# Optimization experiments

Measured on AMD Instinct MI355X. Metric: run time of the kernel, lower is better.

## Reference

```python
import jax, jax.numpy as jnp
import numpy as np

D_MODEL = 1024
NUM_HEADS = 16
HEAD_WIDTH = 64
SEQ_LEN = 2048
BATCH = 2
NEG_INF = -1e9


def alibi_slopes(num_heads):
    # 2**(-i * 8/num_heads) for i = 1..num_heads, shape [H, 1, 1]
    step = 8.0 / num_heads
    i = jnp.arange(1, num_heads + 1, dtype=jnp.float32)
    return (2.0 ** (-i * step))[:, None, None]


def relative_positions(t_q, t_v):
    # matrix[i, j] = j - i, shape [t_q, t_v]
    return (jnp.arange(t_v)[None, :] - jnp.arange(t_q)[:, None]).astype(jnp.float32)


def setup_inputs() -> dict:
    key = jax.random.key(0)
    ks = jax.random.split(key, 6)
    queries = jax.random.normal(ks[0], (BATCH, SEQ_LEN, D_MODEL), dtype=jnp.float32)
    keys = jax.random.normal(ks[1], (BATCH, SEQ_LEN, D_MODEL), dtype=jnp.float32)
    values = jax.random.normal(ks[2], (BATCH, SEQ_LEN, D_MODEL), dtype=jnp.float32)
    # causal additive mask, broadcastable [1, 1, S, S]
    causal = jnp.where(
        jnp.arange(SEQ_LEN)[None, :] > jnp.arange(SEQ_LEN)[:, None], NEG_INF, 0.0
    ).astype(jnp.float32)[None, None]
    scale = 1.0 / np.sqrt(D_MODEL)
    Wq = jax.random.normal(ks[3], (D_MODEL, D_MODEL), dtype=jnp.float32) * scale
    Wk = jax.random.normal(ks[4], (D_MODEL, D_MODEL), dtype=jnp.float32) * scale
    Wv = jax.random.normal(ks[5], (D_MODEL, D_MODEL), dtype=jnp.float32) * scale
    return {"queries": queries, "keys": keys, "values": values, "mask": causal,
            "Wq": Wq, "Wk": Wk, "Wv": Wv}


def reference(queries, keys, values, mask, Wq, Wk, Wv):
    N, t_q, d = queries.shape
    _, t_v, _ = keys.shape
    H, hw = NUM_HEADS, HEAD_WIDTH

    def split_heads(x, t):
        # [N, t, d] -> [N, H, t, hw]  (nn.Linear: x @ W.T)
        return x.reshape(N, t, H, hw).transpose(0, 2, 1, 3)

    q = split_heads(queries @ Wq.T, t_q)
    k = split_heads(keys @ Wk.T, t_v)
    v = split_heads(values @ Wv.T, t_v)

    att = jnp.einsum("bhqd,bhkd->bhqk", q, k) / np.sqrt(hw)
    # ALiBi bias: slope_h * (j - i), broadcast over batch
    att = att + (alibi_slopes(H) * relative_positions(t_q, t_v))[None]
    att = att + mask[:, :, :t_q, :t_v]
    att = jax.nn.softmax(att, axis=-1)
    res = jnp.einsum("bhqk,bhkd->bhqd", att, v)  # [N, H, t_q, hw]
    return res.transpose(0, 2, 1, 3).reshape(N, t_v, d)
```

## Files before the change

### kernel.cpp

```cpp
#include <hip/hip_runtime.h>
#include <hip/hip_bf16.h>

#define BATCH 2
#define HEADS 16
#define SEQ 2048
#define HW 64
#define DMODEL 1024

typedef unsigned short u16;
typedef __attribute__((ext_vector_type(8))) short short8;
typedef __attribute__((ext_vector_type(4))) float floatx4;

typedef __attribute__((address_space(3))) void* lds_t;
typedef const __attribute__((address_space(1))) void* gbl_t;

__device__ __forceinline__ u16 f2bf(float f) {
    union { float f; unsigned int u; } v; v.f = f;
    unsigned int r = v.u + 0x7fffu + ((v.u >> 16) & 1u);
    return (u16)(r >> 16);
}

__device__ __forceinline__ unsigned int pk2bf(float a, float b) {
    union { __hip_bfloat162 h; unsigned int u; } c;
    c.h = __float22bfloat162_rn(make_float2(a, b));
    return c.u;
}

__global__ __launch_bounds__(256) void proj_kernel(
    const float* __restrict__ Xk, const float* __restrict__ Xv, const float* __restrict__ Xq,
    const float* __restrict__ Wk, const float* __restrict__ Wv, const float* __restrict__ Wq,
    u16* __restrict__ Ok, u16* __restrict__ Ov, u16* __restrict__ Oq)
{
    const float* X; const float* W;
    if (blockIdx.z == 0)      { X = Xk; W = Wk; }
    else if (blockIdx.z == 1) { X = Xv; W = Wv; }
    else                      { X = Xq; W = Wq; }

    __shared__ u16 As[128][72];
    __shared__ u16 Bs[128][72];

    const int tid = threadIdx.x;
    const int lane = tid & 63, wave = tid >> 6;
    const int quad = lane >> 4, l15 = lane & 15;
    const int wm = (wave >> 1) << 6, wn = (wave & 1) << 6;
    const int tm = blockIdx.y, tn = blockIdx.x;

    const int sr = tid >> 4;
    const int sc = (tid & 15) << 2;
    const float* Xp = X + (size_t)(tm * 128 + sr) * DMODEL + sc;
    const float* Wp = W + (size_t)(tn * 128 + sr) * DMODEL + sc;

    float4 ra[8], rb[8];
#define PLOAD(K0) \
    for (int i = 0; i < 8; i++) { \
        ra[i] = *reinterpret_cast<const float4*>(Xp + (size_t)16 * i * DMODEL + (K0)); \
        rb[i] = *reinterpret_cast<const float4*>(Wp + (size_t)16 * i * DMODEL + (K0)); \
    }

    floatx4 acc[4][4];
    for (int i = 0; i < 4; i++) for (int j = 0; j < 4; j++) acc[i][j] = (floatx4)0.0f;

    PLOAD(0);
    for (int k0 = 0; k0 < DMODEL; k0 += 64) {
        for (int i = 0; i < 8; i++) {
            uint2 pa; pa.x = pk2bf(ra[i].x, ra[i].y); pa.y = pk2bf(ra[i].z, ra[i].w);
            *reinterpret_cast<uint2*>(&As[sr + 16 * i][sc]) = pa;
            uint2 pb; pb.x = pk2bf(rb[i].x, rb[i].y); pb.y = pk2bf(rb[i].z, rb[i].w);
            *reinterpret_cast<uint2*>(&Bs[sr + 16 * i][sc]) = pb;
        }
        __syncthreads();
        if (k0 + 64 < DMODEL) { PLOAD(k0 + 64); }
        for (int kc = 0; kc < 2; kc++) {
            short8 af[4], bf[4];
            for (int i = 0; i < 4; i++)
                af[i] = *reinterpret_cast<const short8*>(&As[wm + i * 16 + l15][kc * 32 + quad * 8]);
            for (int j = 0; j < 4; j++)
                bf[j] = *reinterpret_cast<const short8*>(&Bs[wn + j * 16 + l15][kc * 32 + quad * 8]);
            for (int i = 0; i < 4; i++)
                for (int j = 0; j < 4; j++)
                    acc[i][j] = __builtin_amdgcn_mfma_f32_16x16x32_bf16(af[i], bf[j], acc[i][j], 0, 0, 0);
        }
        __syncthreads();
    }
#undef PLOAD

    if (blockIdx.z != 1) {
        u16* O = (blockIdx.z == 0) ? Ok : Oq;
        const float mul = (blockIdx.z == 0) ? 1.0f : 0.125f;
        for (int i = 0; i < 4; i++) for (int j = 0; j < 4; j++) {
            int n = (tn << 7) + wn + (j << 4) + l15;
            int h = n >> 6, d = n & 63;
            for (int r = 0; r < 4; r++) {
                int m = (tm << 7) + wm + (i << 4) + (quad << 2) + r;
                int b = m >> 11, s = m & 2047;
                int pc = (((d >> 3) ^ (s & 7)) << 3) | (d & 7);
                O[(size_t)((((b << 4) + h) << 11) + s) * 64 + pc] = f2bf(acc[i][j][r] * mul);
            }
        }
    } else {
        for (int i = 0; i < 4; i++) for (int j = 0; j < 4; j++) {
            int n = (tn << 7) + wn + (j << 4) + l15;
            int h = n >> 6, d = n & 63;
            int m = (tm << 7) + wm + (i << 4) + (quad << 2);
            int b = m >> 11, s0 = m & 2047;
            int ps = (s0 & ~63) | (((((s0 >> 3) & 7) ^ (d & 7)) << 3)) | (s0 & 7);
            uint2 pk;
            pk.x = pk2bf(acc[i][j][0], acc[i][j][1]);
            pk.y = pk2bf(acc[i][j][2], acc[i][j][3]);
            *reinterpret_cast<uint2*>(Ov + ((size_t)(((b << 4) + h) << 6) + d) * SEQ + ps) = pk;
        }
    }
}

__global__ __launch_bounds__(256) void attn_kernel(
    const u16* __restrict__ Qg, const u16* __restrict__ K,
    const u16* __restrict__ VtG, float* __restrict__ out)
{
    __shared__ u16 smem[16896];
    u16* Pst = smem + 12288;

    const int tid = threadIdx.x;
    const int lane = tid & 63, wave = tid >> 6;
    const int quad = lane >> 4, l15 = lane & 15;

    const int bid = blockIdx.x;
    const int qt = 31 - (bid >> 5);
    const int bh = bid & 31;
    const int b = bh >> 4, h = bh & 15;
    const float slope = exp2f(-0.5f * (float)(h + 1));
    const int q0 = qt << 6;
    const int swz = l15 & 7;

    const u16* Qh  = Qg  + (size_t)bh * SEQ * HW;
    const u16* Kh  = K   + (size_t)bh * SEQ * HW;
    const u16* Vth = VtG + (size_t)bh * HW * SEQ;

#define ISSUE_K(KV, BUF) do { \
    const u16* gk_ = Kh + (size_t)((KV) + wave * 16) * 64 + lane * 8; \
    __builtin_amdgcn_global_load_lds((gbl_t)gk_, (lds_t)(smem + (BUF) * 4096 + wave * 1024), 16, 0, 0); \
    __builtin_amdgcn_global_load_lds((gbl_t)(gk_ + 512), (lds_t)(smem + (BUF) * 4096 + wave * 1024 + 512), 16, 0, 0); \
} while (0)
#define ISSUE_V(KV) do { \
    const u16* gv_ = Vth + (size_t)(wave * 16 + (lane >> 3)) * SEQ + (KV) + (lane & 7) * 8; \
    __builtin_amdgcn_global_load_lds((gbl_t)gv_, (lds_t)(smem + 8192 + wave * 1024), 16, 0, 0); \
    __builtin_amdgcn_global_load_lds((gbl_t)(gv_ + 8 * SEQ), (lds_t)(smem + 8192 + wave * 1024 + 512), 16, 0, 0); \
} while (0)

    {
        const u16* gq = Qh + (size_t)(q0 + wave * 16) * 64 + lane * 8;
        __builtin_amdgcn_global_load_lds((gbl_t)gq, (lds_t)(smem + 8192 + wave * 1024), 16, 0, 0);
        __builtin_amdgcn_global_load_lds((gbl_t)(gq + 512), (lds_t)(smem + 8192 + wave * 1024 + 512), 16, 0, 0);
    }
    asm volatile("s_waitcnt vmcnt(0)" ::: "memory");
    short8 qf[2];
    qf[0] = *reinterpret_cast<const short8*>(smem + 8192 + (wave * 16 + l15) * 64 + ((quad ^ swz) << 3));
    qf[1] = *reinterpret_cast<const short8*>(smem + 8192 + (wave * 16 + l15) * 64 + (((quad + 4) ^ swz) << 3));
    asm volatile("s_waitcnt lgkmcnt(0)" ::: "memory");
    __builtin_amdgcn_sched_barrier(0);

    ISSUE_K(0, 0);

    const float L2E = 1.44269504088896340736f;
    const float MB  = 12.0f * L2E;
    const int qg = q0 + (wave << 4) + l15;
    const float SL = slope * L2E;

    float lpart = 0.0f;
    floatx4 acc_o[4];
    for (int t = 0; t < 4; t++) acc_o[t] = (floatx4)0.0f;

    for (int kt = 0; kt <= qt; kt++) {
        const int kv0 = kt << 6;
        asm volatile("s_waitcnt vmcnt(0)" ::: "memory");
        __builtin_amdgcn_s_barrier();
        __builtin_amdgcn_sched_barrier(0);
        ISSUE_V(kv0);
        if (kt < qt) { ISSUE_K(kv0 + 64, (kt + 1) & 1); }

        const u16* Kbase = smem + (kt & 1) * 4096;
        floatx4 sv[4];
        __builtin_amdgcn_s_setprio(1);
        for (int t = 0; t < 4; t++) {
            short8 kf0 = *reinterpret_cast<const short8*>(Kbase + (t * 16 + l15) * 64 + ((quad ^ swz) << 3));
            short8 kf1 = *reinterpret_cast<const short8*>(Kbase + (t * 16 + l15) * 64 + (((quad + 4) ^ swz) << 3));
            floatx4 s = (floatx4)0.0f;
            s = __builtin_amdgcn_mfma_f32_16x16x32_bf16(kf0, qf[0], s, 0, 0, 0);
            s = __builtin_amdgcn_mfma_f32_16x16x32_bf16(kf1, qf[1], s, 0, 0, 0);
            sv[t] = s;
        }
        __builtin_amdgcn_s_setprio(0);

        u16* Pt = Pst + wave * 1152;
        if (kt < qt) {
            const float b0 = fmaf(SL, (float)(kv0 + (quad << 2) - qg), -MB);
            for (int t = 0; t < 4; t++) {
                float p0 = __builtin_amdgcn_exp2f(fmaf(sv[t][0], L2E, fmaf(SL, (float)(t * 16 + 0), b0)));
                float p1 = __builtin_amdgcn_exp2f(fmaf(sv[t][1], L2E, fmaf(SL, (float)(t * 16 + 1), b0)));
                float p2 = __builtin_amdgcn_exp2f(fmaf(sv[t][2], L2E, fmaf(SL, (float)(t * 16 + 2), b0)));
                float p3 = __builtin_amdgcn_exp2f(fmaf(sv[t][3], L2E, fmaf(SL, (float)(t * 16 + 3), b0)));
                lpart += (p0 + p1) + (p2 + p3);
                uint2 pk; pk.x = pk2bf(p0, p1); pk.y = pk2bf(p2, p3);
                *reinterpret_cast<uint2*>(Pt + l15 * 72 + t * 16 + (quad << 2)) = pk;
            }
        } else {
            const float fb = (float)(kv0 + (quad << 2) - qg);
            for (int t = 0; t < 4; t++) {
                float p[4];
                for (int r = 0; r < 4; r++) {
                    float rel = fb + (float)(t * 16 + r);
                    float bd = fmaf(fminf(slope * rel, -1e9f * rel), L2E, -MB);
                    p[r] = __builtin_amdgcn_exp2f(fmaf(sv[t][r], L2E, bd));
                }
                lpart += (p[0] + p[1]) + (p[2] + p[3]);
                uint2 pk; pk.x = pk2bf(p[0], p[1]); pk.y = pk2bf(p[2], p[3]);
                *reinterpret_cast<uint2*>(Pt + l15 * 72 + t * 16 + (quad << 2)) = pk;
            }
        }

        if (kt < qt) { asm volatile("s_waitcnt vmcnt(2)" ::: "memory"); }
        else         { asm volatile("s_waitcnt vmcnt(0)" ::: "memory"); }
        __builtin_amdgcn_s_barrier();
        __builtin_amdgcn_sched_barrier(0);

        short8 pf0 = *reinterpret_cast<const short8*>(Pt + l15 * 72 + quad * 8);
        short8 pf1 = *reinterpret_cast<const short8*>(Pt + l15 * 72 + 32 + quad * 8);
        __builtin_amdgcn_s_setprio(1);
        for (int t2 = 0; t2 < 4; t2++) {
            short8 vf0 = *reinterpret_cast<const short8*>(smem + 8192 + (t2 * 16 + l15) * 64 + ((quad ^ swz) << 3));
            short8 vf1 = *reinterpret_cast<const short8*>(smem + 8192 + (t2 * 16 + l15) * 64 + (((quad + 4) ^ swz) << 3));
            acc_o[t2] = __builtin_amdgcn_mfma_f32_16x16x32_bf16(vf0, pf0, acc_o[t2], 0, 0, 0);
            acc_o[t2] = __builtin_amdgcn_mfma_f32_16x16x32_bf16(vf1, pf1, acc_o[t2], 0, 0, 0);
        }
        __builtin_amdgcn_s_setprio(0);
    }
#undef ISSUE_K
#undef ISSUE_V

    float l_run = lpart;
    l_run += __shfl_xor(l_run, 16);
    l_run += __shfl_xor(l_run, 32);
    const float inv = 1.0f / l_run;

    float* op = out + (size_t)(b * SEQ + qg) * DMODEL + h * 64;
    for (int t2 = 0; t2 < 4; t2++) {
        float4 o;
        o.x = acc_o[t2][0] * inv; o.y = acc_o[t2][1] * inv;
        o.z = acc_o[t2][2] * inv; o.w = acc_o[t2][3] * inv;
        *reinterpret_cast<float4*>(op + t2 * 16 + (quad << 2)) = o;
    }
}

extern "C" void kernel_launch(void* const* d_in, const int* in_sizes, int n_in,
                              void* d_out, int out_size, void* d_ws, size_t ws_size,
                              hipStream_t stream) {
    const float* q  = (const float*)d_in[0];
    const float* k  = (const float*)d_in[1];
    const float* v  = (const float*)d_in[2];
    const float* wq = (const float*)d_in[4];
    const float* wk = (const float*)d_in[5];
    const float* wv = (const float*)d_in[6];
    float* out = (float*)d_out;

    const size_t headElems = (size_t)BATCH * HEADS * SEQ * HW;
    u16* Kb  = (u16*)d_ws;
    u16* VtB = Kb + headElems;
    u16* Qb  = VtB + headElems;

    dim3 pgrid(DMODEL / 128, (BATCH * SEQ) / 128, 3);
    proj_kernel<<<pgrid, 256, 0, stream>>>(k, v, q, wk, wv, wq, Kb, VtB, Qb);
    attn_kernel<<<BATCH * HEADS * (SEQ / 64), 256, 0, stream>>>(Qb, Kb, VtB, out);
}
```

Measured before the change: 206.6 us.

## Pre-convert inputs and weights to bf16 and use direct-to-LDS projection GEMM

Adds a conversion kernel that casts activations and weights to bf16 in one pass, folding the 0.125 query scale into Wq. The bf16 tensors go into spare workspace and the output buffer. A new projection GEMM then reads bf16 operands through global_load_lds into XOR-swizzled LDS tiles without padding, aiming to halve GEMM load traffic and remove per-tile conversion work. The cost is an extra launch and a full read/write pass over all inputs. It depends on the workspace being large enough, falling back to the old f32 projection otherwise, and may double-scale Q if the attention kernel already applies the scale.

```diff
diff --git a/kernel.cpp b/kernel.cpp
--- a/kernel.cpp
+++ b/kernel.cpp
@@ -26,7 +26,119 @@
     return c.u;
 }
 
-__global__ __launch_bounds__(256) void proj_kernel(
+__global__ __launch_bounds__(256) void conv_kernel(
+    const float* __restrict__ s0, const float* __restrict__ s1, const float* __restrict__ s2,
+    const float* __restrict__ s3, const float* __restrict__ s4, const float* __restrict__ s5,
+    u16* __restrict__ d0, u16* __restrict__ d1, u16* __restrict__ d2,
+    u16* __restrict__ d3, u16* __restrict__ d4, u16* __restrict__ d5)
+{
+    const int z = blockIdx.y;
+    const float* src; u16* dst; int n; float mul = 1.0f;
+    if (z == 0)      { src = s0; dst = d0; n = BATCH * SEQ * DMODEL; }
+    else if (z == 1) { src = s1; dst = d1; n = BATCH * SEQ * DMODEL; }
+    else if (z == 2) { src = s2; dst = d2; n = BATCH * SEQ * DMODEL; }
+    else if (z == 3) { src = s3; dst = d3; n = DMODEL * DMODEL; }
+    else if (z == 4) { src = s4; dst = d4; n = DMODEL * DMODEL; }
+    else             { src = s5; dst = d5; n = DMODEL * DMODEL; mul = 0.125f; }
+
+    const int i0 = (blockIdx.x * 256 + threadIdx.x) * 8;
+    const int stride = gridDim.x * 256 * 8;
+    for (int i = i0; i < n; i += stride) {
+        float4 a = *reinterpret_cast<const float4*>(src + i);
+        float4 b = *reinterpret_cast<const float4*>(src + i + 4);
+        uint4 o;
+        o.x = pk2bf(a.x * mul, a.y * mul);
+        o.y = pk2bf(a.z * mul, a.w * mul);
+        o.z = pk2bf(b.x * mul, b.y * mul);
+        o.w = pk2bf(b.z * mul, b.w * mul);
+        *reinterpret_cast<uint4*>(dst + i) = o;
+    }
+}
+
+__global__ __launch_bounds__(256) void proj_bf16_kernel(
+    const u16* __restrict__ Xk, const u16* __restrict__ Xv, const u16* __restrict__ Xq,
+    const u16* __restrict__ Wk, const u16* __restrict__ Wv, const u16* __restrict__ Wq,
+    u16* __restrict__ Ok, u16* __restrict__ Ov, u16* __restrict__ Oq)
+{
+    const u16* X; const u16* W;
+    if (blockIdx.z == 0)      { X = Xk; W = Wk; }
+    else if (blockIdx.z == 1) { X = Xv; W = Wv; }
+    else                      { X = Xq; W = Wq; }
+
+    __shared__ u16 As[128][64];
+    __shared__ u16 Bs[128][64];
+
+    const int tid = threadIdx.x;
+    const int lane = tid & 63, wave = tid >> 6;
+    const int quad = lane >> 4, l15 = lane & 15;
+    const int swz = l15 & 7;
+    const int wm = (wave >> 1) << 6, wn = (wave & 1) << 6;
+    const int tm = blockIdx.y, tn = blockIdx.x;
+
+    const int srow = (wave << 5) + (lane >> 3);
+    const int scol = (((lane & 7) ^ (lane >> 3)) << 3);
+    const u16* gA = X + (size_t)(tm * 128 + srow) * DMODEL + scol;
+    const u16* gB = W + (size_t)(tn * 128 + srow) * DMODEL + scol;
+
+    floatx4 acc[4][4];
+    for (int i = 0; i < 4; i++) for (int j = 0; j < 4; j++) acc[i][j] = (floatx4)0.0f;
+
+    for (int k0 = 0; k0 < DMODEL; k0 += 64) {
+        for (int j = 0; j < 4; j++) {
+            __builtin_amdgcn_global_load_lds((gbl_t)(gA + (size_t)j * 8 * DMODEL + k0),
+                (lds_t)(&As[(wave << 5) + (j << 3)][0]), 16, 0, 0);
+            __builtin_amdgcn_global_load_lds((gbl_t)(gB + (size_t)j * 8 * DMODEL + k0),
+                (lds_t)(&Bs[(wave << 5) + (j << 3)][0]), 16, 0, 0);
+        }
+        __syncthreads();
+        {
+            short8 af[4], bf[4];
+            for (int i = 0; i < 4; i++)
+                af[i] = *reinterpret_cast<const short8*>(&As[wm + i * 16 + l15][(quad ^ swz) << 3]);
+            for (int j = 0; j < 4; j++)
+                bf[j] = *reinterpret_cast<const short8*>(&Bs[wn + j * 16 + l15][(quad ^ swz) << 3]);
+            for (int i = 0; i < 4; i++)
+                for (int j = 0; j < 4; j++)
+                    acc[i][j] = __builtin_amdgcn_mfma_f32_16x16x32_bf16(af[i], bf[j], acc[i][j], 0, 0, 0);
+            for (int i = 0; i < 4; i++)
+                af[i] = *reinterpret_cast<const short8*>(&As[wm + i * 16 + l15][((quad + 4) ^ swz) << 3]);
+            for (int j = 0; j < 4; j++)
+                bf[j] = *reinterpret_cast<const short8*>(&Bs[wn + j * 16 + l15][((quad + 4) ^ swz) << 3]);
+            for (int i = 0; i < 4; i++)
+                for (int j = 0; j < 4; j++)
+                    acc[i][j] = __builtin_amdgcn_mfma_f32_16x16x32_bf16(af[i], bf[j], acc[i][j], 0, 0, 0);
+        }
+        __syncthreads();
+    }
+
+    if (blockIdx.z != 1) {
+        u16* O = (blockIdx.z == 0) ? Ok : Oq;
+        for (int i = 0; i < 4; i++) for (int j = 0; j < 4; j++) {
+            int n = (tn << 7) + wn + (j << 4) + l15;
+            int h = n >> 6, d = n & 63;
+            for (int r = 0; r < 4; r++) {
+                int m = (tm << 7) + wm + (i << 4) + (quad << 2) + r;
+                int b = m >> 11, s = m & 2047;
+                int pc = (((d >> 3) ^ (s & 7)) << 3) | (d & 7);
+                O[(size_t)((((b << 4) + h) << 11) + s) * 64 + pc] = f2bf(acc[i][j][r]);
+            }
+        }
+    } else {
+        for (int i = 0; i < 4; i++) for (int j = 0; j < 4; j++) {
+            int n = (tn << 7) + wn + (j << 4) + l15;
+            int h = n >> 6, d = n & 63;
+            int m = (tm << 7) + wm + (i << 4) + (quad << 2);
+            int b = m >> 11, s0 = m & 2047;
+            int ps = (s0 & ~63) | (((((s0 >> 3) & 7) ^ (d & 7)) << 3)) | (s0 & 7);
+            uint2 pk;
+            pk.x = pk2bf(acc[i][j][0], acc[i][j][1]);
+            pk.y = pk2bf(acc[i][j][2], acc[i][j][3]);
+            *reinterpret_cast<uint2*>(Ov + ((size_t)(((b << 4) + h) << 6) + d) * SEQ + ps) = pk;
+        }
+    }
+}
+
+__global__ __launch_bounds__(256) void proj_f32_kernel(
     const float* __restrict__ Xk, const float* __restrict__ Xv, const float* __restrict__ Xq,
     const float* __restrict__ Wk, const float* __restrict__ Wv, const float* __restrict__ Wq,
     u16* __restrict__ Ok, u16* __restrict__ Ov, u16* __restrict__ Oq)
@@ -261,12 +373,29 @@
     const float* wv = (const float*)d_in[6];
     float* out = (float*)d_out;
 
-    const size_t headElems = (size_t)BATCH * HEADS * SEQ * HW;
+    const size_t he = (size_t)BATCH * HEADS * SEQ * HW;
+    const size_t we = (size_t)DMODEL * DMODEL;
     u16* Kb  = (u16*)d_ws;
-    u16* VtB = Kb + headElems;
-    u16* Qb  = VtB + headElems;
-
-    dim3 pgrid(DMODEL / 128, (BATCH * SEQ) / 128, 3);
-    proj_kernel<<<pgrid, 256, 0, stream>>>(k, v, q, wk, wv, wq, Kb, VtB, Qb);
+    u16* VtB = Kb + he;
+    u16* Qb  = VtB + he;
+
+    const size_t need_A = (size_t)(6 * he) * sizeof(u16);
+    const bool pathA = (ws_size >= need_A) && ((size_t)out_size >= 3 * we * sizeof(u16));
+
+    if (pathA) {
+        u16* Xkb = Qb + he;
+        u16* Xvb = Xkb + he;
+        u16* Xqb = Xvb + he;
+        u16* Wkb = (u16*)d_out;
+        u16* Wvb = Wkb + we;
+        u16* Wqb = Wvb + we;
+        conv_kernel<<<dim3(512, 6), 256, 0, stream>>>(k, v, q, wk, wv, wq,
+                                                      Xkb, Xvb, Xqb, Wkb, Wvb, Wqb);
+        proj_bf16_kernel<<<dim3(DMODEL / 128, (BATCH * SEQ) / 128, 3), 256, 0, stream>>>(
+            Xkb, Xvb, Xqb, Wkb, Wvb, Wqb, Kb, VtB, Qb);
+    } else {
+        proj_f32_kernel<<<dim3(DMODEL / 128, (BATCH * SEQ) / 128, 3), 256, 0, stream>>>(
+            k, v, q, wk, wv, wq, Kb, VtB, Qb);
+    }
     attn_kernel<<<BATCH * HEADS * (SEQ / 64), 256, 0, stream>>>(Qb, Kb, VtB, out);
 }
```

Result: no change. 207.7 us (+0.5%).

## Pre-convert weights to bf16 and stream them into LDS via direct global loads

Applied to the files above, without the earlier changes.

Adds a small kernel that converts the three weight matrices to bf16 once per call, folding the 1/8 query scale into Wq, and stages them in the output buffer as scratch. The projection GEMM then loads the bf16 weight tile straight into LDS with global_load_lds using an XOR-swizzled layout, instead of loading fp32 weights per tile and converting them in registers. The grid is flattened and remapped so row tiles are grouped per XCD for better L2 reuse. This halves weight traffic and frees VGPRs, at the cost of an extra kernel launch and a weight-conversion pass.

```diff
diff --git a/kernel.cpp b/kernel.cpp
--- a/kernel.cpp
+++ b/kernel.cpp
@@ -26,47 +26,75 @@
     return c.u;
 }
 
+__global__ __launch_bounds__(256) void convw_kernel(
+    const float* __restrict__ wk, const float* __restrict__ wv, const float* __restrict__ wq,
+    u16* __restrict__ ok, u16* __restrict__ ov, u16* __restrict__ oq)
+{
+    const int z = blockIdx.y;
+    const float* src; u16* dst; float mul = 1.0f;
+    if (z == 0)      { src = wk; dst = ok; }
+    else if (z == 1) { src = wv; dst = ov; }
+    else             { src = wq; dst = oq; mul = 0.125f; }
+
+    const int i = (blockIdx.x * 256 + threadIdx.x) * 8;
+    float4 a = *reinterpret_cast<const float4*>(src + i);
+    float4 b = *reinterpret_cast<const float4*>(src + i + 4);
+    uint4 o;
+    o.x = pk2bf(a.x * mul, a.y * mul);
+    o.y = pk2bf(a.z * mul, a.w * mul);
+    o.z = pk2bf(b.x * mul, b.y * mul);
+    o.w = pk2bf(b.z * mul, b.w * mul);
+    *reinterpret_cast<uint4*>(dst + i) = o;
+}
+
 __global__ __launch_bounds__(256) void proj_kernel(
     const float* __restrict__ Xk, const float* __restrict__ Xv, const float* __restrict__ Xq,
-    const float* __restrict__ Wk, const float* __restrict__ Wv, const float* __restrict__ Wq,
+    const u16* __restrict__ Wb,
     u16* __restrict__ Ok, u16* __restrict__ Ov, u16* __restrict__ Oq)
 {
-    const float* X; const float* W;
-    if (blockIdx.z == 0)      { X = Xk; W = Wk; }
-    else if (blockIdx.z == 1) { X = Xv; W = Wv; }
-    else                      { X = Xq; W = Wq; }
+    const int bid = blockIdx.x;
+    const int xcd = bid & 7, idx = bid >> 3;
+    const int z = idx >> 5;
+    const int r = idx & 31;
+    const int tm = (xcd << 2) | (r >> 3);
+    const int tn = r & 7;
+
+    const float* X = (z == 0) ? Xk : (z == 1) ? Xv : Xq;
+    const u16* W = Wb + (size_t)z * DMODEL * DMODEL;
 
     __shared__ u16 As[128][72];
-    __shared__ u16 Bs[128][72];
+    __shared__ u16 Bs[128][64];
 
     const int tid = threadIdx.x;
     const int lane = tid & 63, wave = tid >> 6;
     const int quad = lane >> 4, l15 = lane & 15;
+    const int swz = l15 & 7;
     const int wm = (wave >> 1) << 6, wn = (wave & 1) << 6;
-    const int tm = blockIdx.y, tn = blockIdx.x;
 
     const int sr = tid >> 4;
     const int sc = (tid & 15) << 2;
     const float* Xp = X + (size_t)(tm * 128 + sr) * DMODEL + sc;
-    const float* Wp = W + (size_t)(tn * 128 + sr) * DMODEL + sc;
-
-    float4 ra[8], rb[8];
+
+    const int srowB = (wave << 5) + (lane >> 3);
+    const int scolB = (((lane & 7) ^ (lane >> 3)) << 3);
+    const u16* gB = W + (size_t)(tn * 128 + srowB) * DMODEL + scolB;
+
+    float4 ra[8];
 #define PLOAD(K0) \
-    for (int i = 0; i < 8; i++) { \
-        ra[i] = *reinterpret_cast<const float4*>(Xp + (size_t)16 * i * DMODEL + (K0)); \
-        rb[i] = *reinterpret_cast<const float4*>(Wp + (size_t)16 * i * DMODEL + (K0)); \
-    }
+    for (int i = 0; i < 8; i++) \
+        ra[i] = *reinterpret_cast<const float4*>(Xp + (size_t)16 * i * DMODEL + (K0));
 
     floatx4 acc[4][4];
     for (int i = 0; i < 4; i++) for (int j = 0; j < 4; j++) acc[i][j] = (floatx4)0.0f;
 
     PLOAD(0);
     for (int k0 = 0; k0 < DMODEL; k0 += 64) {
+        for (int j = 0; j < 4; j++)
+            __builtin_amdgcn_global_load_lds((gbl_t)(gB + (size_t)j * 8 * DMODEL + k0),
+                (lds_t)(&Bs[(wave << 5) + (j << 3)][0]), 16, 0, 0);
         for (int i = 0; i < 8; i++) {
             uint2 pa; pa.x = pk2bf(ra[i].x, ra[i].y); pa.y = pk2bf(ra[i].z, ra[i].w);
             *reinterpret_cast<uint2*>(&As[sr + 16 * i][sc]) = pa;
-            uint2 pb; pb.x = pk2bf(rb[i].x, rb[i].y); pb.y = pk2bf(rb[i].z, rb[i].w);
-            *reinterpret_cast<uint2*>(&Bs[sr + 16 * i][sc]) = pb;
         }
         __syncthreads();
         if (k0 + 64 < DMODEL) { PLOAD(k0 + 64); }
@@ -75,7 +103,7 @@
             for (int i = 0; i < 4; i++)
                 af[i] = *reinterpret_cast<const short8*>(&As[wm + i * 16 + l15][kc * 32 + quad * 8]);
             for (int j = 0; j < 4; j++)
-                bf[j] = *reinterpret_cast<const short8*>(&Bs[wn + j * 16 + l15][kc * 32 + quad * 8]);
+                bf[j] = *reinterpret_cast<const short8*>(&Bs[wn + j * 16 + l15][((kc * 4 + quad) ^ swz) << 3]);
             for (int i = 0; i < 4; i++)
                 for (int j = 0; j < 4; j++)
                     acc[i][j] = __builtin_amdgcn_mfma_f32_16x16x32_bf16(af[i], bf[j], acc[i][j], 0, 0, 0);
@@ -84,17 +112,16 @@
     }
 #undef PLOAD
 
-    if (blockIdx.z != 1) {
-        u16* O = (blockIdx.z == 0) ? Ok : Oq;
-        const float mul = (blockIdx.z == 0) ? 1.0f : 0.125f;
+    if (z != 1) {
+        u16* O = (z == 0) ? Ok : Oq;
         for (int i = 0; i < 4; i++) for (int j = 0; j < 4; j++) {
             int n = (tn << 7) + wn + (j << 4) + l15;
             int h = n >> 6, d = n & 63;
-            for (int r = 0; r < 4; r++) {
-                int m = (tm << 7) + wm + (i << 4) + (quad << 2) + r;
+            for (int rr = 0; rr < 4; rr++) {
+                int m = (tm << 7) + wm + (i << 4) + (quad << 2) + rr;
                 int b = m >> 11, s = m & 2047;
                 int pc = (((d >> 3) ^ (s & 7)) << 3) | (d & 7);
-                O[(size_t)((((b << 4) + h) << 11) + s) * 64 + pc] = f2bf(acc[i][j][r] * mul);
+                O[(size_t)((((b << 4) + h) << 11) + s) * 64 + pc] = f2bf(acc[i][j][rr]);
             }
         }
     } else {
@@ -261,12 +288,14 @@
     const float* wv = (const float*)d_in[6];
     float* out = (float*)d_out;
 
-    const size_t headElems = (size_t)BATCH * HEADS * SEQ * HW;
+    const size_t he = (size_t)BATCH * HEADS * SEQ * HW;
+    const size_t we = (size_t)DMODEL * DMODEL;
     u16* Kb  = (u16*)d_ws;
-    u16* VtB = Kb + headElems;
-    u16* Qb  = VtB + headElems;
-
-    dim3 pgrid(DMODEL / 128, (BATCH * SEQ) / 128, 3);
-    proj_kernel<<<pgrid, 256, 0, stream>>>(k, v, q, wk, wv, wq, Kb, VtB, Qb);
+    u16* VtB = Kb + he;
+    u16* Qb  = VtB + he;
+
+    u16* Wb = (u16*)d_out;
+    convw_kernel<<<dim3(512, 3), 256, 0, stream>>>(wk, wv, wq, Wb, Wb + we, Wb + 2 * we);
+    proj_kernel<<<768, 256, 0, stream>>>(k, v, q, Wb, Kb, VtB, Qb);
     attn_kernel<<<BATCH * HEADS * (SEQ / 64), 256, 0, stream>>>(Qb, Kb, VtB, out);
 }
```

Result: faster. 184.6 us, median of 4 (-10.7%).
